# Optimization experiments

Hardware: AMD Instinct MI355X
Metric: run time of the kernel (lower is better)

The kernel has to match this reference:

```python
import jax, jax.numpy as jnp
import numpy as np
import math

B, S, D, H, L, V, MAXLEN = 4, 2047, 256, 8, 2, 32000, 2048
DK = D // H
DFF = 2 * D
EPS = 1e-5


def make_pe(max_len, d):
    pos = jnp.arange(max_len, dtype=jnp.float32)[:, None]
    div = jnp.exp(jnp.arange(0, d, 2, dtype=jnp.float32) * (-math.log(10000.0) / d))
    pe = jnp.zeros((max_len, d), dtype=jnp.float32)
    pe = pe.at[:, 0::2].set(jnp.sin(pos * div))
    pe = pe.at[:, 1::2].set(jnp.cos(pos * div))
    return pe[None]  # [1, max_len, d]


def setup_inputs() -> dict:
    key = jax.random.key(0)
    ks = jax.random.split(key, 16)
    s = 0.02
    T = S + 1
    return {
        "embeddings": jax.random.normal(ks[0], (B, D), jnp.float32),
        "output_tokens": jax.random.randint(ks[1], (B, S), 0, V, jnp.int64),
        "causal_mask": jnp.tril(jnp.ones((T, T), jnp.int32))[None, None],  # [1,1,T,T]
        "key_padding_mask": jnp.ones((B, 1, 1, T), jnp.int32),
        "tok_emb": jax.random.normal(ks[2], (V, D), jnp.float32) * s,
        "pe": make_pe(MAXLEN, D),
        "Wq": jax.random.normal(ks[3], (L, D, D), jnp.float32) * s,
        "Wk": jax.random.normal(ks[4], (L, D, D), jnp.float32) * s,
        "Wv": jax.random.normal(ks[5], (L, D, D), jnp.float32) * s,
        "Wo": jax.random.normal(ks[6], (L, D, D), jnp.float32) * s,
        "bo": jnp.zeros((L, D), jnp.float32),
        "ln1_g": jnp.ones((L, D), jnp.float32),
        "ln1_b": jnp.zeros((L, D), jnp.float32),
        "W1": jax.random.normal(ks[7], (L, D, DFF), jnp.float32) * s,
        "b1": jnp.zeros((L, DFF), jnp.float32),
        "W2": jax.random.normal(ks[8], (L, DFF, D), jnp.float32) * s,
        "b2": jnp.zeros((L, D), jnp.float32),
        "ln2_g": jnp.ones((L, D), jnp.float32),
        "ln2_b": jnp.zeros((L, D), jnp.float32),
    }


def layer_norm(x, g, b):
    mu = jnp.mean(x, axis=-1, keepdims=True)
    var = jnp.mean(jnp.square(x - mu), axis=-1, keepdims=True)
    return (x - mu) * jax.lax.rsqrt(var + EPS) * g + b


def attention(x, Wq, Wk, Wv, Wo, bo, causal_mask, key_padding_mask):
    b, t, d = x.shape
    q = (x @ Wq).reshape(b, t, H, DK)
    k = (x @ Wk).reshape(b, t, H, DK)
    v = (x @ Wv).reshape(b, t, H, DK)
    scores = jnp.einsum('bqhd,bkhd->bhqk', q, k) / math.sqrt(DK)  # [B,H,T,T]
    neg = jnp.float32(-jnp.inf)
    scores = jnp.where(causal_mask == 0, neg, scores)
    scores = jnp.where(key_padding_mask == 0, neg, scores)
    attn = jax.nn.softmax(scores, axis=-1)
    out = jnp.einsum('bhqk,bkhd->bqhd', attn, v).reshape(b, t, d)
    return out @ Wo + bo


def reference(embeddings, output_tokens, causal_mask, key_padding_mask,
              tok_emb, pe, Wq, Wk, Wv, Wo, bo, ln1_g, ln1_b,
              W1, b1, W2, b2, ln2_g, ln2_b):
    emb_tok = tok_emb[output_tokens]                       # [B,S,D]
    x = jnp.concatenate([embeddings[:, None, :], emb_tok], axis=1)  # [B,T,D]
    x = x + pe[:, :x.shape[1]]
    for l in range(L):
        a = attention(x, Wq[l], Wk[l], Wv[l], Wo[l], bo[l], causal_mask, key_padding_mask)
        x = layer_norm(x + a, ln1_g[l], ln1_b[l])
        ff = jax.nn.relu(x @ W1[l] + b1[l]) @ W2[l] + b2[l]
        x = layer_norm(x + ff, ln2_g[l], ln2_b[l])
    return x[:, 1:, :]  # drop the prepended embedding position
```

## Files before the change

### kernel.cpp

```cpp
#include <hip/hip_runtime.h>
#include <cstdint>
#include <cstddef>

#define B_   4
#define S_   2047
#define T_   2048
#define D_   256
#define H_   8
#define DK_  32
#define DFF_ 512
#define L_   2

typedef short          s8v  __attribute__((ext_vector_type(8)));
typedef float          f4v  __attribute__((ext_vector_type(4)));
typedef unsigned short u4v  __attribute__((ext_vector_type(4)));
typedef unsigned short u8v  __attribute__((ext_vector_type(8)));
typedef unsigned int   u2v  __attribute__((ext_vector_type(2)));
typedef unsigned int   uint32;

union U8 { u8v v; unsigned short e[8]; };

__device__ __forceinline__ float bf2f(unsigned short h) {
    unsigned int u = ((unsigned int)h) << 16;
    float f; __builtin_memcpy(&f, &u, 4); return f;
}
__device__ __forceinline__ unsigned short f2bf(float f) {
    unsigned int u; __builtin_memcpy(&u, &f, 4);
    u += 0x7fffu + ((u >> 16) & 1u);
    return (unsigned short)(u >> 16);
}
__device__ __forceinline__ uint32 pack_bf2(float lo, float hi) {
    uint32 a, b;
    __builtin_memcpy(&a, &lo, 4); __builtin_memcpy(&b, &hi, 4);
    a += 0x8000u; b += 0x8000u;
    return __builtin_amdgcn_perm(b, a, 0x07060302);
}

#define QSCALE 0.1767766952966369f

__global__ __launch_bounds__(256) void embed_k(
    const float* __restrict__ emb, const int* __restrict__ toks,
    const float* __restrict__ tokE, const float* __restrict__ pe,
    unsigned short* __restrict__ X)
{
    int idx = blockIdx.x * 256 + threadIdx.x;
    int d8 = (idx & 31) * 8;
    int t  = (idx >> 5) & (T_ - 1);
    int b  = idx >> 16;
    const float* src = (t == 0) ? (emb + b * D_)
                                : (tokE + (size_t)toks[b * S_ + t - 1] * D_);
    const float* p = pe + (size_t)t * D_ + d8;
    U8 o;
#pragma unroll
    for (int j = 0; j < 8; ++j) o.e[j] = f2bf(src[d8 + j] + p[j]);
    *(u8v*)(X + (size_t)(b * T_ + t) * D_ + d8) = o.v;
}

__global__ __launch_bounds__(256) void tr_all_k(
    const float* __restrict__ Wq, const float* __restrict__ Wk,
    const float* __restrict__ Wv, const float* __restrict__ Wo,
    const float* __restrict__ W1, const float* __restrict__ W2,
    unsigned short* __restrict__ WqkvT, unsigned short* __restrict__ WoT,
    unsigned short* __restrict__ W1T, unsigned short* __restrict__ W2T)
{
    __shared__ float tile[32][33];
    int idx = blockIdx.x;
    const float* src; unsigned short* dst; int R, C, tr, tc;
    if (idx < 512) {
        int w = idx >> 7, rem = idx & 127, l = rem >> 6, t = rem & 63;
        tr = t >> 3; tc = t & 7; R = 256; C = 256;
        src = (w == 0 ? Wq : w == 1 ? Wk : w == 2 ? Wv : Wo) + (size_t)l * 65536;
        dst = (w < 3) ? WqkvT + (size_t)l * 196608 + (size_t)w * 65536
                      : WoT + (size_t)l * 65536;
    } else if (idx < 768) {
        int rem = idx - 512, l = rem >> 7, t = rem & 127;
        tr = t >> 4; tc = t & 15; R = 256; C = 512;
        src = W1 + (size_t)l * 131072; dst = W1T + (size_t)l * 131072;
    } else {
        int rem = idx - 768, l = rem >> 7, t = rem & 127;
        tr = t >> 3; tc = t & 7; R = 512; C = 256;
        src = W2 + (size_t)l * 131072; dst = W2T + (size_t)l * 131072;
    }
    int x = threadIdx.x & 31, y = threadIdx.x >> 5;
    int r0 = tr * 32, c0 = tc * 32;
#pragma unroll
    for (int i = 0; i < 32; i += 8) tile[y + i][x] = src[(size_t)(r0 + y + i) * C + c0 + x];
    __syncthreads();
#pragma unroll
    for (int i = 0; i < 32; i += 8)
        dst[(size_t)(c0 + y + i) * R + r0 + x] = f2bf(tile[x][y + i]);
}

__global__ __launch_bounds__(256) void gemm64_k(
    const unsigned short* __restrict__ A, const unsigned short* __restrict__ WT,
    const float* __restrict__ bias,
    unsigned short* __restrict__ oq, unsigned short* __restrict__ ok,
    unsigned short* __restrict__ ov, unsigned short* __restrict__ out,
    int K, int Ntot, int mode)
{
    __shared__ unsigned short At[64 * 72];
    __shared__ unsigned short Wt[64 * 72];
    const int tid = threadIdx.x;
    const int wave = tid >> 6, lane = tid & 63, l15 = lane & 15, quad = lane >> 4;
    const int m0 = blockIdx.x * 64, n0g = blockIdx.y * 64;

    f4v acc[4];
#pragma unroll
    for (int i = 0; i < 4; ++i) acc[i] = (f4v){0.f, 0.f, 0.f, 0.f};

    const int arow = tid >> 2, acg = (tid & 3) * 16;
    const unsigned short* ag = A + (size_t)(m0 + arow) * K + acg;
    const unsigned short* wg = WT + (size_t)(n0g + arow) * K + acg;
    u8v a0 = *(const u8v*)ag, a1 = *(const u8v*)(ag + 8);
    u8v w0 = *(const u8v*)wg, w1 = *(const u8v*)(wg + 8);

    const int niter = K >> 6;
    for (int kk = 0; kk < niter; ++kk) {
        *(u8v*)&At[arow * 72 + acg] = a0; *(u8v*)&At[arow * 72 + acg + 8] = a1;
        *(u8v*)&Wt[arow * 72 + acg] = w0; *(u8v*)&Wt[arow * 72 + acg + 8] = w1;
        __syncthreads();
        if (kk + 1 < niter) {
            int o = (kk + 1) * 64;
            a0 = *(const u8v*)(ag + o); a1 = *(const u8v*)(ag + o + 8);
            w0 = *(const u8v*)(wg + o); w1 = *(const u8v*)(wg + o + 8);
        }
#pragma unroll
        for (int ks = 0; ks < 2; ++ks) {
            s8v aF = *(const s8v*)&At[(wave * 16 + l15) * 72 + ks * 32 + quad * 8];
#pragma unroll
            for (int nt = 0; nt < 4; ++nt) {
                s8v wF = *(const s8v*)&Wt[(nt * 16 + l15) * 72 + ks * 32 + quad * 8];
                acc[nt] = __builtin_amdgcn_mfma_f32_16x16x32_bf16(aF, wF, acc[nt], 0, 0, 0);
            }
        }
        __syncthreads();
    }

    const int b = m0 >> 11, t0 = m0 & (T_ - 1);
    if (mode == 0) {
        int sub = blockIdx.y >> 2;
        int cb  = (blockIdx.y & 3) * 64;
        if (sub < 2) {
            unsigned short* dst = sub ? ok : oq;
            float sc = sub ? 1.f : QSCALE;
#pragma unroll
            for (int nt = 0; nt < 4; ++nt) {
                int c = cb + nt * 16 + l15, hh = c >> 5, dk = c & 31;
#pragma unroll
                for (int r = 0; r < 4; ++r) {
                    int t = t0 + wave * 16 + quad * 4 + r;
                    dst[((size_t)(b * H_ + hh) * T_ + t) * DK_ + dk] = f2bf(acc[nt][r] * sc);
                }
            }
        } else {
            unsigned short* Vb = At;
#pragma unroll
            for (int nt = 0; nt < 4; ++nt) {
                int base = (nt * 16 + l15) * 72 + wave * 16 + quad * 4;
                *(uint32*)&Vb[base]     = pack_bf2(acc[nt][0], acc[nt][1]);
                *(uint32*)&Vb[base + 2] = pack_bf2(acc[nt][2], acc[nt][3]);
            }
            __syncthreads();
            int c = tid >> 2, chunk = tid & 3;
            int cg = cb + c, hh = cg >> 5, dk = cg & 31;
            unsigned short* dst = ov + ((size_t)(b * H_ + hh) * DK_ + dk) * T_ + t0 + chunk * 16;
            u8v v0 = *(u8v*)&Vb[c * 72 + chunk * 16];
            u8v v1 = *(u8v*)&Vb[c * 72 + chunk * 16 + 8];
            *(u8v*)dst = v0; *(u8v*)(dst + 8) = v1;
        }
    } else {
#pragma unroll
        for (int nt = 0; nt < 4; ++nt) {
            int c = n0g + nt * 16 + l15;
            float bv = bias[c];
#pragma unroll
            for (int r = 0; r < 4; ++r) {
                float v = acc[nt][r] + bv;
                v = v > 0.f ? v : 0.f;
                out[(size_t)(m0 + wave * 16 + quad * 4 + r) * Ntot + c] = f2bf(v);
            }
        }
    }
}

__global__ __launch_bounds__(256) void gemm16_k(
    const unsigned short* __restrict__ A, const unsigned short* __restrict__ WT,
    const float* __restrict__ bias, const unsigned short* __restrict__ resid,
    const float* __restrict__ gamma, const float* __restrict__ beta,
    unsigned short* __restrict__ out, int K)
{
    __shared__ unsigned short At[16 * 72];
    __shared__ unsigned short Wt[256 * 72];
    const int tid = threadIdx.x;
    const int wave = tid >> 6, lane = tid & 63, l15 = lane & 15, quad = lane >> 4;
    const int m0 = blockIdx.x * 16;

    f4v acc[4];
#pragma unroll
    for (int i = 0; i < 4; ++i) acc[i] = (f4v){0.f, 0.f, 0.f, 0.f};

    const int arow = tid >> 4, ac4 = (tid & 15) * 4;
    const unsigned short* ag = A + (size_t)(m0 + arow) * K + ac4;
    const unsigned short* wg = WT + (size_t)tid * K;
    u4v aR = *(const u4v*)ag;
    u8v wR[8];
#pragma unroll
    for (int j = 0; j < 8; ++j) wR[j] = *(const u8v*)(wg + j * 8);

    const int niter = K >> 6;
    for (int kk = 0; kk < niter; ++kk) {
        *(u4v*)&At[arow * 72 + ac4] = aR;
#pragma unroll
        for (int j = 0; j < 8; ++j) *(u8v*)&Wt[tid * 72 + j * 8] = wR[j];
        __syncthreads();
        if (kk + 1 < niter) {
            int o = (kk + 1) * 64;
            aR = *(const u4v*)(ag + o);
#pragma unroll
            for (int j = 0; j < 8; ++j) wR[j] = *(const u8v*)(wg + o + j * 8);
        }
#pragma unroll
        for (int ks = 0; ks < 2; ++ks) {
            s8v aF = *(const s8v*)&At[l15 * 72 + ks * 32 + quad * 8];
#pragma unroll
            for (int nt = 0; nt < 4; ++nt) {
                s8v wF = *(const s8v*)&Wt[(wave * 64 + nt * 16 + l15) * 72 + ks * 32 + quad * 8];
                acc[nt] = __builtin_amdgcn_mfma_f32_16x16x32_bf16(aF, wF, acc[nt], 0, 0, 0);
            }
        }
        __syncthreads();
    }

    const int rbase = quad * 4;
    float* LNs = (float*)Wt;
    float* LNq = LNs + 64;
    float ps[4] = {0, 0, 0, 0}, pq[4] = {0, 0, 0, 0};
#pragma unroll
    for (int nt = 0; nt < 4; ++nt) {
        int c = wave * 64 + nt * 16 + l15;
        float bv = bias[c];
#pragma unroll
        for (int r = 0; r < 4; ++r) {
            float v = acc[nt][r] + bv + bf2f(resid[(size_t)(m0 + rbase + r) * D_ + c]);
            acc[nt][r] = v;
            ps[r] += v; pq[r] += v * v;
        }
    }
#pragma unroll
    for (int r = 0; r < 4; ++r) {
        float s = ps[r], q = pq[r];
        s += __shfl_xor(s, 1); q += __shfl_xor(q, 1);
        s += __shfl_xor(s, 2); q += __shfl_xor(q, 2);
        s += __shfl_xor(s, 4); q += __shfl_xor(q, 4);
        s += __shfl_xor(s, 8); q += __shfl_xor(q, 8);
        if (l15 == 0) { LNs[(rbase + r) * 4 + wave] = s; LNq[(rbase + r) * 4 + wave] = q; }
    }
    __syncthreads();
    float mu[4], rsig[4];
#pragma unroll
    for (int r = 0; r < 4; ++r) {
        int row = rbase + r;
        float s = LNs[row * 4] + LNs[row * 4 + 1] + LNs[row * 4 + 2] + LNs[row * 4 + 3];
        float q = LNq[row * 4] + LNq[row * 4 + 1] + LNq[row * 4 + 2] + LNq[row * 4 + 3];
        float m = s * (1.f / 256.f);
        mu[r] = m;
        rsig[r] = rsqrtf(q * (1.f / 256.f) - m * m + 1e-5f);
    }
#pragma unroll
    for (int nt = 0; nt < 4; ++nt) {
        int c = wave * 64 + nt * 16 + l15;
        float g = gamma[c], be = beta[c];
#pragma unroll
        for (int r = 0; r < 4; ++r)
            out[(size_t)(m0 + rbase + r) * D_ + c] =
                f2bf((acc[nt][r] - mu[r]) * rsig[r] * g + be);
    }
}

__global__ __launch_bounds__(256) void attn_k(
    const unsigned short* __restrict__ Qh, const unsigned short* __restrict__ Kh,
    const unsigned short* __restrict__ VT, unsigned short* __restrict__ AO)
{
    __shared__ unsigned short Kt[128 * 40];
    __shared__ unsigned short Vt[32 * 144];
    __shared__ unsigned short Ps[4][16 * 136];

    const int tid = threadIdx.x, wave = tid >> 6, lane = tid & 63;
    const int l15 = lane & 15, quad = lane >> 4;
    const int bh = blockIdx.y, b = bh >> 3, h = bh & 7;
    const size_t hoff = (size_t)bh * T_ * DK_;
    unsigned short* Pw = &Ps[wave][0];

    const int qts[2] = { (int)blockIdx.x, 31 - (int)blockIdx.x };
    const int nk0 = qts[0] / 2 + 1, nk1 = qts[1] / 2 + 1;
    const int ntot = nk0 + nk1;

    const int krow = tid >> 1, khalf = (tid & 1) * 16;
    const int vdk = tid >> 3, vc = (tid & 7) * 16;
    const unsigned short* kgp = Kh + hoff + (size_t)krow * DK_ + khalf;
    const unsigned short* vgp = VT + ((size_t)bh * DK_ + vdk) * T_ + vc;

    u8v kr0 = *(const u8v*)kgp, kr1 = *(const u8v*)(kgp + 8);
    u8v vr0 = *(const u8v*)vgp, vr1 = *(const u8v*)(vgp + 8);

    s8v qB = {0,0,0,0,0,0,0,0};
    f4v O0 = {0,0,0,0}, O1 = {0,0,0,0};
    float m_i = -1e30f, l_i = 0.f;
    int nkt = 0, q0w = 0;

    for (int it = 0; it < ntot; ++it) {
        const int phase = (it >= nk0);
        const int kt = phase ? it - nk0 : it;
        if (kt == 0) {
            int qt = qts[phase]; nkt = phase ? nk1 : nk0;
            q0w = qt * 64 + wave * 16;
            qB = *(const s8v*)(Qh + hoff + (size_t)(q0w + l15) * DK_ + quad * 8);
            O0 = (f4v){0,0,0,0}; O1 = (f4v){0,0,0,0};
            m_i = -1e30f; l_i = 0.f;
        }
        *(u8v*)&Kt[krow * 40 + khalf]     = kr0;
        *(u8v*)&Kt[krow * 40 + khalf + 8] = kr1;
        *(u8v*)&Vt[vdk * 144 + vc]        = vr0;
        *(u8v*)&Vt[vdk * 144 + vc + 8]    = vr1;
        __syncthreads();
        {
            int itn = it + 1;
            if (itn < ntot) {
                int ktn = (itn >= nk0) ? itn - nk0 : itn;
                const unsigned short* kn = kgp + (size_t)ktn * 128 * DK_;
                const unsigned short* vn = vgp + (size_t)ktn * 128;
                kr0 = *(const u8v*)kn; kr1 = *(const u8v*)(kn + 8);
                vr0 = *(const u8v*)vn; vr1 = *(const u8v*)(vn + 8);
            }
        }
        const int k0 = kt * 128;

        f4v s[8];
        f4v zero = {0,0,0,0};
#pragma unroll
        for (int nt = 0; nt < 8; ++nt) {
            s8v kA = *(const s8v*)&Kt[(nt * 16 + l15) * 40 + quad * 8];
            s[nt] = __builtin_amdgcn_mfma_f32_16x16x32_bf16(kA, qB, zero, 0, 0, 0);
        }
        if (kt == nkt - 1) {
            int query = q0w + l15;
#pragma unroll
            for (int nt = 0; nt < 8; ++nt)
#pragma unroll
                for (int r = 0; r < 4; ++r) {
                    int key = k0 + nt * 16 + quad * 4 + r;
                    if (key > query) s[nt][r] = -1e30f;
                }
        }
        float mt = -1e30f;
#pragma unroll
        for (int nt = 0; nt < 8; ++nt)
            mt = fmaxf(mt, fmaxf(fmaxf(s[nt][0], s[nt][1]), fmaxf(s[nt][2], s[nt][3])));
        mt = fmaxf(mt, __shfl_xor(mt, 16));
        mt = fmaxf(mt, __shfl_xor(mt, 32));
        float mn = fmaxf(m_i, mt);
        float alpha = __expf(m_i - mn);
        m_i = mn;
        float rs = 0.f;
#pragma unroll
        for (int nt = 0; nt < 8; ++nt)
#pragma unroll
            for (int r = 0; r < 4; ++r) {
                float p = __expf(s[nt][r] - mn);
                s[nt][r] = p;
                rs += p;
            }
        rs += __shfl_xor(rs, 16);
        rs += __shfl_xor(rs, 32);
        l_i = l_i * alpha + rs;
#pragma unroll
        for (int r = 0; r < 4; ++r) {
            float ar = __shfl(alpha, quad * 4 + r);
            O0[r] *= ar; O1[r] *= ar;
        }
#pragma unroll
        for (int nt = 0; nt < 8; ++nt) {
            u2v pw;
            pw.x = pack_bf2(s[nt][0], s[nt][1]);
            pw.y = pack_bf2(s[nt][2], s[nt][3]);
            *(u2v*)&Pw[l15 * 136 + nt * 16 + quad * 4] = pw;
        }
#pragma unroll
        for (int ks = 0; ks < 4; ++ks) {
            s8v aP = *(const s8v*)&Pw[l15 * 136 + ks * 32 + quad * 8];
            s8v v0 = *(const s8v*)&Vt[l15 * 144 + ks * 32 + quad * 8];
            s8v v1 = *(const s8v*)&Vt[(16 + l15) * 144 + ks * 32 + quad * 8];
            O0 = __builtin_amdgcn_mfma_f32_16x16x32_bf16(aP, v0, O0, 0, 0, 0);
            O1 = __builtin_amdgcn_mfma_f32_16x16x32_bf16(aP, v1, O1, 0, 0, 0);
        }
        if (kt == nkt - 1) {
#pragma unroll
            for (int r = 0; r < 4; ++r) {
                float linv = 1.f / __shfl(l_i, quad * 4 + r);
                int row = q0w + quad * 4 + r;
                size_t base = (size_t)(b * T_ + row) * D_ + h * DK_;
                AO[base + l15]      = f2bf(O0[r] * linv);
                AO[base + 16 + l15] = f2bf(O1[r] * linv);
            }
        }
        __syncthreads();
    }
}

__global__ __launch_bounds__(256) void copyout_k(
    const unsigned short* __restrict__ X, float* __restrict__ out)
{
    int idx = blockIdx.x * 256 + threadIdx.x;
    if (idx >= B_ * S_ * (D_ / 8)) return;
    int d8 = (idx & 31) * 8;
    int s  = (idx >> 5) % S_;
    int b  = (idx >> 5) / S_;
    U8 v; v.v = *(const u8v*)(X + ((size_t)(b * T_ + s + 1)) * D_ + d8);
    float* o = out + ((size_t)b * S_ + s) * D_ + d8;
#pragma unroll
    for (int j = 0; j < 8; ++j) o[j] = bf2f(v.e[j]);
}

extern "C" void kernel_launch(void* const* d_in, const int* in_sizes, int n_in,
                              void* d_out, int out_size, void* d_ws, size_t ws_size,
                              hipStream_t stream)
{
    const float* emb  = (const float*)d_in[0];
    const int*   toks = (const int*)d_in[1];
    const float* tokE = (const float*)d_in[4];
    const float* pe   = (const float*)d_in[5];
    const float* Wq   = (const float*)d_in[6];
    const float* Wk   = (const float*)d_in[7];
    const float* Wv   = (const float*)d_in[8];
    const float* Wo   = (const float*)d_in[9];
    const float* bo   = (const float*)d_in[10];
    const float* g1   = (const float*)d_in[11];
    const float* be1  = (const float*)d_in[12];
    const float* W1   = (const float*)d_in[13];
    const float* b1   = (const float*)d_in[14];
    const float* W2   = (const float*)d_in[15];
    const float* b2   = (const float*)d_in[16];
    const float* g2   = (const float*)d_in[17];
    const float* be2  = (const float*)d_in[18];
    float* out = (float*)d_out;

    unsigned short* ws = (unsigned short*)d_ws;
    size_t off = 0;
    const size_t XSZ = (size_t)B_ * T_ * D_;
    unsigned short* Xa    = ws + off; off += XSZ;
    unsigned short* Xb    = ws + off; off += XSZ;
    unsigned short* Qh    = ws + off; off += XSZ;
    unsigned short* Kh    = ws + off; off += XSZ;
    unsigned short* VTb   = ws + off; off += XSZ;
    unsigned short* AOb   = ws + off; off += XSZ;
    unsigned short* Hb    = ws + off; off += (size_t)B_ * T_ * DFF_;
    unsigned short* WqkvT = ws + off; off += (size_t)L_ * 3 * D_ * D_;
    unsigned short* WoT   = ws + off; off += (size_t)L_ * D_ * D_;
    unsigned short* W1T   = ws + off; off += (size_t)L_ * D_ * DFF_;
    unsigned short* W2T   = ws + off; off += (size_t)L_ * DFF_ * D_;
    (void)ws_size; (void)in_sizes; (void)n_in; (void)out_size;

    embed_k<<<dim3((B_ * T_ * D_ / 8) / 256), 256, 0, stream>>>(emb, toks, tokE, pe, Xa);
    tr_all_k<<<dim3(1024), 256, 0, stream>>>(Wq, Wk, Wv, Wo, W1, W2, WqkvT, WoT, W1T, W2T);

    for (int l = 0; l < L_; ++l) {
        const unsigned short* wqkv = WqkvT + (size_t)l * 3 * D_ * D_;
        const unsigned short* wo   = WoT + (size_t)l * D_ * D_;
        const unsigned short* w1   = W1T + (size_t)l * D_ * DFF_;
        const unsigned short* w2   = W2T + (size_t)l * DFF_ * D_;

        gemm64_k<<<dim3(128, 12), 256, 0, stream>>>(Xa, wqkv, nullptr,
                                                    Qh, Kh, VTb, nullptr, D_, D_, 0);
        attn_k<<<dim3(16, 32), 256, 0, stream>>>(Qh, Kh, VTb, AOb);
        gemm16_k<<<dim3(512), 256, 0, stream>>>(AOb, wo, bo + l * D_, Xa,
                                                g1 + l * D_, be1 + l * D_, Xb, D_);
        gemm64_k<<<dim3(128, 8), 256, 0, stream>>>(Xb, w1, b1 + l * DFF_,
                                                   nullptr, nullptr, nullptr, Hb, D_, DFF_, 1);
        gemm16_k<<<dim3(512), 256, 0, stream>>>(Hb, w2, b2 + l * D_, Xb,
                                                g2 + l * D_, be2 + l * D_, Xa, DFF_);
    }
    copyout_k<<<dim3(1024), 256, 0, stream>>>(Xa, out);
}
```

Measured before the change: 291.2 us.

## Double-buffer attention K/V tiles, use exp2 softmax, merge prep kernels

The attention kernel now double-buffers its K and V shared-memory tiles, which lets it drop the trailing barrier so each iteration needs only one __syncthreads. The Q scale folds in log2(e) so the softmax can use exp2f in place of __expf. The embedding and weight-transpose kernels are merged into a single launch to save one launch. Together these add shared-memory usage (more LDS per block, possibly lower occupancy) and rely on the single barrier being enough to protect the Ps buffer between iterations.

```diff
diff --git a/kernel.cpp b/kernel.cpp
--- a/kernel.cpp
+++ b/kernel.cpp
@@ -36,27 +36,12 @@
     return __builtin_amdgcn_perm(b, a, 0x07060302);
 }
 
-#define QSCALE 0.1767766952966369f
-
-__global__ __launch_bounds__(256) void embed_k(
+#define QSCALE2 0.25503485951542068f
+
+__global__ __launch_bounds__(256) void prep_k(
     const float* __restrict__ emb, const int* __restrict__ toks,
     const float* __restrict__ tokE, const float* __restrict__ pe,
-    unsigned short* __restrict__ X)
-{
-    int idx = blockIdx.x * 256 + threadIdx.x;
-    int d8 = (idx & 31) * 8;
-    int t  = (idx >> 5) & (T_ - 1);
-    int b  = idx >> 16;
-    const float* src = (t == 0) ? (emb + b * D_)
-                                : (tokE + (size_t)toks[b * S_ + t - 1] * D_);
-    const float* p = pe + (size_t)t * D_ + d8;
-    U8 o;
-#pragma unroll
-    for (int j = 0; j < 8; ++j) o.e[j] = f2bf(src[d8 + j] + p[j]);
-    *(u8v*)(X + (size_t)(b * T_ + t) * D_ + d8) = o.v;
-}
-
-__global__ __launch_bounds__(256) void tr_all_k(
+    unsigned short* __restrict__ X,
     const float* __restrict__ Wq, const float* __restrict__ Wk,
     const float* __restrict__ Wv, const float* __restrict__ Wo,
     const float* __restrict__ W1, const float* __restrict__ W2,
@@ -64,7 +49,21 @@
     unsigned short* __restrict__ W1T, unsigned short* __restrict__ W2T)
 {
     __shared__ float tile[32][33];
-    int idx = blockIdx.x;
+    if (blockIdx.x < 1024) {
+        int idx = blockIdx.x * 256 + threadIdx.x;
+        int d8 = (idx & 31) * 8;
+        int t  = (idx >> 5) & (T_ - 1);
+        int b  = idx >> 16;
+        const float* src = (t == 0) ? (emb + b * D_)
+                                    : (tokE + (size_t)toks[b * S_ + t - 1] * D_);
+        const float* p = pe + (size_t)t * D_ + d8;
+        U8 o;
+#pragma unroll
+        for (int j = 0; j < 8; ++j) o.e[j] = f2bf(src[d8 + j] + p[j]);
+        *(u8v*)(X + (size_t)(b * T_ + t) * D_ + d8) = o.v;
+        return;
+    }
+    int idx = blockIdx.x - 1024;
     const float* src; unsigned short* dst; int R, C, tr, tc;
     if (idx < 512) {
         int w = idx >> 7, rem = idx & 127, l = rem >> 6, t = rem & 63;
@@ -142,7 +141,7 @@
         int cb  = (blockIdx.y & 3) * 64;
         if (sub < 2) {
             unsigned short* dst = sub ? ok : oq;
-            float sc = sub ? 1.f : QSCALE;
+            float sc = sub ? 1.f : QSCALE2;
 #pragma unroll
             for (int nt = 0; nt < 4; ++nt) {
                 int c = cb + nt * 16 + l15, hh = c >> 5, dk = c & 31;
@@ -281,8 +280,8 @@
     const unsigned short* __restrict__ Qh, const unsigned short* __restrict__ Kh,
     const unsigned short* __restrict__ VT, unsigned short* __restrict__ AO)
 {
-    __shared__ unsigned short Kt[128 * 40];
-    __shared__ unsigned short Vt[32 * 144];
+    __shared__ unsigned short Kt[2][128 * 40];
+    __shared__ unsigned short Vt[2][32 * 144];
     __shared__ unsigned short Ps[4][16 * 136];
 
     const int tid = threadIdx.x, wave = tid >> 6, lane = tid & 63;
@@ -318,11 +317,12 @@
             O0 = (f4v){0,0,0,0}; O1 = (f4v){0,0,0,0};
             m_i = -1e30f; l_i = 0.f;
         }
-        *(u8v*)&Kt[krow * 40 + khalf]     = kr0;
-        *(u8v*)&Kt[krow * 40 + khalf + 8] = kr1;
-        *(u8v*)&Vt[vdk * 144 + vc]        = vr0;
-        *(u8v*)&Vt[vdk * 144 + vc + 8]    = vr1;
-        __syncthreads();
+        unsigned short* KtC = Kt[it & 1];
+        unsigned short* VtC = Vt[it & 1];
+        *(u8v*)&KtC[krow * 40 + khalf]     = kr0;
+        *(u8v*)&KtC[krow * 40 + khalf + 8] = kr1;
+        *(u8v*)&VtC[vdk * 144 + vc]        = vr0;
+        *(u8v*)&VtC[vdk * 144 + vc + 8]    = vr1;
         {
             int itn = it + 1;
             if (itn < ntot) {
@@ -333,13 +333,14 @@
                 vr0 = *(const u8v*)vn; vr1 = *(const u8v*)(vn + 8);
             }
         }
+        __syncthreads();
         const int k0 = kt * 128;
 
         f4v s[8];
         f4v zero = {0,0,0,0};
 #pragma unroll
         for (int nt = 0; nt < 8; ++nt) {
-            s8v kA = *(const s8v*)&Kt[(nt * 16 + l15) * 40 + quad * 8];
+            s8v kA = *(const s8v*)&KtC[(nt * 16 + l15) * 40 + quad * 8];
             s[nt] = __builtin_amdgcn_mfma_f32_16x16x32_bf16(kA, qB, zero, 0, 0, 0);
         }
         if (kt == nkt - 1) {
@@ -359,14 +360,14 @@
         mt = fmaxf(mt, __shfl_xor(mt, 16));
         mt = fmaxf(mt, __shfl_xor(mt, 32));
         float mn = fmaxf(m_i, mt);
-        float alpha = __expf(m_i - mn);
+        float alpha = exp2f(m_i - mn);
         m_i = mn;
         float rs = 0.f;
 #pragma unroll
         for (int nt = 0; nt < 8; ++nt)
 #pragma unroll
             for (int r = 0; r < 4; ++r) {
-                float p = __expf(s[nt][r] - mn);
+                float p = exp2f(s[nt][r] - mn);
                 s[nt][r] = p;
                 rs += p;
             }
@@ -388,8 +389,8 @@
 #pragma unroll
         for (int ks = 0; ks < 4; ++ks) {
             s8v aP = *(const s8v*)&Pw[l15 * 136 + ks * 32 + quad * 8];
-            s8v v0 = *(const s8v*)&Vt[l15 * 144 + ks * 32 + quad * 8];
-            s8v v1 = *(const s8v*)&Vt[(16 + l15) * 144 + ks * 32 + quad * 8];
+            s8v v0 = *(const s8v*)&VtC[l15 * 144 + ks * 32 + quad * 8];
+            s8v v1 = *(const s8v*)&VtC[(16 + l15) * 144 + ks * 32 + quad * 8];
             O0 = __builtin_amdgcn_mfma_f32_16x16x32_bf16(aP, v0, O0, 0, 0, 0);
             O1 = __builtin_amdgcn_mfma_f32_16x16x32_bf16(aP, v1, O1, 0, 0, 0);
         }
@@ -403,7 +404,6 @@
                 AO[base + 16 + l15] = f2bf(O1[r] * linv);
             }
         }
-        __syncthreads();
     }
 }
 
@@ -460,8 +460,9 @@
     unsigned short* W2T   = ws + off; off += (size_t)L_ * DFF_ * D_;
     (void)ws_size; (void)in_sizes; (void)n_in; (void)out_size;
 
-    embed_k<<<dim3((B_ * T_ * D_ / 8) / 256), 256, 0, stream>>>(emb, toks, tokE, pe, Xa);
-    tr_all_k<<<dim3(1024), 256, 0, stream>>>(Wq, Wk, Wv, Wo, W1, W2, WqkvT, WoT, W1T, W2T);
+    prep_k<<<dim3(2048), 256, 0, stream>>>(emb, toks, tokE, pe, Xa,
+                                           Wq, Wk, Wv, Wo, W1, W2,
+                                           WqkvT, WoT, W1T, W2T);
 
     for (int l = 0; l < L_; ++l) {
         const unsigned short* wqkv = WqkvT + (size_t)l * 3 * D_ * D_;
```

Result: slower. 301.2 us (+3.4%).
